# Optimization experiments

Measured on AMD Instinct MI355X. Metric: run time of the kernel, lower is better.

The kernel has to match this reference:

```python
import jax, jax.numpy as jnp
import numpy as np

B = 16          # batch
DF = 1536       # dinov2 feature dim
D = 1024        # projected dim (32*32)
V = 6890        # SMPL vertices (hard-coded in DECO)
PD = 256        # vertex positional-embedding dim
HID = 512       # feature_transform hidden dim
C = 133         # semantic contact classes


def setup_inputs() -> dict:
    key = jax.random.key(0)
    ks = jax.random.split(key, 16)
    s = 0.02
    n = lambda k, shp: s * jax.random.normal(k, shp, dtype=jnp.float32)
    return {
        "features": jax.random.normal(ks[0], (B, DF), dtype=jnp.float32),
        "W_scene": n(ks[1], (DF, D)), "b_scene": jnp.zeros((D,), jnp.float32),
        "W_contact": n(ks[2], (DF, D)), "b_contact": jnp.zeros((D,), jnp.float32),
        "Wq": n(ks[3], (D, D)), "Wk": n(ks[4], (D, D)),
        "Wv": n(ks[5], (D, D)), "Wo": n(ks[6], (D, D)),
        "W_cls": n(ks[7], (D, V)), "b_cls": jnp.zeros((V,), jnp.float32),
        "pos_emb": n(ks[8], (V, PD)),
        "W_ft1": n(ks[9], (D + PD, HID)), "b_ft1": jnp.zeros((HID,), jnp.float32),
        "W_ft2": n(ks[10], (HID, C)), "b_ft2": jnp.zeros((C,), jnp.float32),
    }


def reference(features, W_scene, b_scene, W_contact, b_contact,
              Wq, Wk, Wv, Wo, W_cls, b_cls, pos_emb,
              W_ft1, b_ft1, W_ft2, b_ft2):
    b = features.shape[0]
    # projectors (dinov2 branch)
    sem = features @ W_scene + b_scene          # [B, D]
    part = features @ W_contact + b_contact     # [B, D]
    # cross attention over seq-len-1 tokens: q from sem, k/v from part
    q = (sem @ Wq)[:, None, :]                  # [B, 1, D]
    k = (part @ Wk)[:, None, :]
    v = (part @ Wv)[:, None, :]
    scores = jnp.einsum('bqd,bkd->bqk', q, k) / jnp.sqrt(jnp.float32(D))
    w = jax.nn.softmax(scores, axis=-1)
    att = jnp.einsum('bqk,bkd->bqd', w, v) @ Wo  # [B, 1, D]
    # per-vertex contact probability
    cont = jax.nn.sigmoid(att[:, 0, :] @ W_cls + b_cls)  # [B, V]
    # shared semantic classifier: the torch code loops over batches, does
    # nonzero() on (cont > 0.5), gathers pos embeddings for contact vertices,
    # runs feature_transform, and scatters into zeros(B, C, V). The masked
    # vectorized form below computes identical values.
    mask = cont > 0.5                           # [B, V] (int constant wrt grad)
    att_bv = jnp.broadcast_to(att, (b, V, D))   # att[b] repeated per vertex
    pos_bv = jnp.broadcast_to(pos_emb[None], (b, V, PD))
    combined = jnp.concatenate([att_bv, pos_bv], axis=-1)   # [B, V, D+PD]
    h = jax.nn.relu(combined @ W_ft1 + b_ft1)   # [B, V, HID]
    preds = h @ W_ft2 + b_ft2                   # [B, V, C]
    semantic_cont = jnp.where(mask[:, None, :],
                              jnp.transpose(preds, (0, 2, 1)),
                              jnp.float32(0.0))  # [B, C, V]
    return (cont, semantic_cont)
```

## Files before the change

### kernel.cpp

```cpp
#include <hip/hip_runtime.h>
#include <hip/hip_bf16.h>

#define B_   16
#define DF_  1536
#define D_   1024
#define V_   6890
#define PD_  256
#define HID_ 512
#define C_   133
#define VPAD 6912
#define CPAD 144

typedef short short8 __attribute__((ext_vector_type(8)));
typedef float float4_ __attribute__((ext_vector_type(4)));
typedef unsigned short ushort_t;

#define MFMA16 __builtin_amdgcn_mfma_f32_16x16x32_bf16

__device__ __forceinline__ float b2f(ushort_t u) {
  union { unsigned int i; float f; } x;
  x.i = ((unsigned int)u) << 16;
  return x.f;
}
__device__ __forceinline__ ushort_t f2b(float f) {
  union { float f; unsigned int i; } x;
  x.f = f;
  unsigned int r = (x.i + 0x7fffu + ((x.i >> 16) & 1u)) >> 16;
  return (ushort_t)r;
}
__device__ __forceinline__ unsigned int f22u(float h0, float h1) {
  __hip_bfloat162 hb = __float22bfloat162_rn(make_float2(h0, h1));
  unsigned int u;
  __builtin_memcpy(&u, &hb, sizeof(u));
  return u;
}

__global__ __launch_bounds__(256) void k_gemv_fA(const float* __restrict__ A,
                                                 const float* __restrict__ W,
                                                 const float* __restrict__ bias,
                                                 double* __restrict__ outd,
                                                 float* __restrict__ outf,
                                                 int K, int N) {
  __shared__ double sA[DF_];
  int b = blockIdx.y;
  for (int i = threadIdx.x; i < K; i += 256) sA[i] = (double)A[b * K + i];
  __syncthreads();
  int jl = threadIdx.x & 15, ks = threadIdx.x >> 4;
  int j  = blockIdx.x * 16 + jl;
  int klen = K >> 4;
  const double* Ar = sA + ks * klen;
  const float*  Wp = W + (size_t)(ks * klen) * N + j;
  double acc = 0.0;
#pragma unroll 8
  for (int kk = 0; kk < klen; ++kk)
    acc += Ar[kk] * (double)Wp[(size_t)kk * N];
  __shared__ double red[16][16];
  red[ks][jl] = acc;
  __syncthreads();
  if (threadIdx.x < 16) {
    int jj = blockIdx.x * 16 + threadIdx.x;
    double s = 0.0;
#pragma unroll
    for (int q = 0; q < 16; ++q) s += red[q][threadIdx.x];
    if (bias) s += (double)bias[jj];
    if (outd) outd[b * N + jj] = s;
    if (outf) outf[b * N + jj] = (float)s;
  }
}

__global__ __launch_bounds__(256) void k_gemv_dA(const double* __restrict__ A,
                                                 const float* __restrict__ W,
                                                 const float* __restrict__ bias,
                                                 double* __restrict__ outd,
                                                 float* __restrict__ outf,
                                                 int K, int N) {
  __shared__ double sA[D_];
  int b = blockIdx.y;
  for (int i = threadIdx.x; i < K; i += 256) sA[i] = A[b * K + i];
  __syncthreads();
  int jl = threadIdx.x & 15, ks = threadIdx.x >> 4;
  int j  = blockIdx.x * 16 + jl;
  int klen = K >> 4;
  const double* Ar = sA + ks * klen;
  const float*  Wp = W + (size_t)(ks * klen) * N + j;
  double acc = 0.0;
#pragma unroll 8
  for (int kk = 0; kk < klen; ++kk)
    acc += Ar[kk] * (double)Wp[(size_t)kk * N];
  __shared__ double red[16][16];
  red[ks][jl] = acc;
  __syncthreads();
  if (threadIdx.x < 16) {
    int jj = blockIdx.x * 16 + threadIdx.x;
    double s = 0.0;
#pragma unroll
    for (int q = 0; q < 16; ++q) s += red[q][threadIdx.x];
    if (bias) s += (double)bias[jj];
    if (outd) outd[b * N + jj] = s;
    if (outf) outf[b * N + jj] = (float)s;
  }
}

__global__ __launch_bounds__(256) void k_cont(const double* __restrict__ att,
                                              const float* __restrict__ Wcls,
                                              const float* __restrict__ bcls,
                                              unsigned char* __restrict__ maskb,
                                              float* __restrict__ out0) {
  int vl = threadIdx.x & 15, ks = threadIdx.x >> 4;
  int v  = blockIdx.x * 16 + vl;
  int vc = v < V_ ? v : V_ - 1;
  double acc[B_];
#pragma unroll
  for (int b = 0; b < B_; ++b) acc[b] = 0.0;
  int k0 = ks * 64;
#pragma unroll 8
  for (int kk = 0; kk < 64; ++kk) {
    int k = k0 + kk;
    double w = (double)Wcls[(size_t)k * V_ + vc];
#pragma unroll
    for (int b = 0; b < B_; ++b) acc[b] += att[b * D_ + k] * w;
  }
  __shared__ double red[16][B_][16];
#pragma unroll
  for (int b = 0; b < B_; ++b) red[ks][b][vl] = acc[b];
  __syncthreads();
  int b = threadIdx.x >> 4;
  double s = 0.0;
#pragma unroll
  for (int q = 0; q < 16; ++q) s += red[q][b][vl];
  if (v < V_) {
    s += (double)bcls[v];
    maskb[b * V_ + v] = (s > 0.0) ? 1 : 0;
    out0[b * V_ + v] = (float)(1.0 / (1.0 + exp(-s)));
  }
}

__global__ __launch_bounds__(256) void k_prep(const float* __restrict__ Wft2,
                                              const float* __restrict__ Wft1,
                                              const float* __restrict__ pos,
                                              ushort_t* __restrict__ WT,
                                              ushort_t* __restrict__ WbT,
                                              ushort_t* __restrict__ PB) {
  int i = blockIdx.x * 256 + threadIdx.x;
  if (i < CPAD * HID_) {
    int c = i >> 9, k = i & (HID_ - 1);
    WT[i] = (c < C_) ? f2b(Wft2[(size_t)k * C_ + c]) : (ushort_t)0;
    return;
  }
  i -= CPAD * HID_;
  if (i < HID_ * PD_) {
    int k = i & (HID_ - 1), pd = i >> 9;
    WbT[(size_t)k * PD_ + pd] = f2b(Wft1[(size_t)(D_ + pd) * HID_ + k]);
    return;
  }
  i -= HID_ * PD_;
  if (i < V_ * PD_) PB[i] = f2b(pos[i]);
}

__global__ __launch_bounds__(256) void k_pproj(const ushort_t* __restrict__ PB,
                                               const ushort_t* __restrict__ WbT,
                                               ushort_t* __restrict__ PP) {
  int wave = threadIdx.x >> 6, lane = threadIdx.x & 63;
  int q = lane >> 4, l15 = lane & 15;
  int m0 = blockIdx.x * 64 + wave * 16;
  int n0 = blockIdx.y * 64;
  int vc = m0 + l15; vc = vc < V_ ? vc : V_ - 1;
  const ushort_t* pb = PB + (size_t)vc * PD_;
  float4_ acc[4] = {};
#pragma unroll 2
  for (int kt = 0; kt < 8; ++kt) {
    int jb = kt * 32 + q * 8;
    short8 a = *(const short8*)(pb + jb);
#pragma unroll
    for (int nf = 0; nf < 4; ++nf) {
      int n = n0 + nf * 16 + l15;
      short8 bfr = *(const short8*)(WbT + (size_t)n * PD_ + jb);
      acc[nf] = MFMA16(a, bfr, acc[nf], 0, 0, 0);
    }
  }
  int v0w = m0 + q * 4;
#pragma unroll
  for (int nf = 0; nf < 4; ++nf)
#pragma unroll
    for (int r = 0; r < 4; ++r)
      PP[(size_t)(v0w + r) * HID_ + (n0 + nf * 16 + l15)] = f2b(acc[nf][r]);
}

__global__ __launch_bounds__(256, 2) void k_main(const ushort_t* __restrict__ WT,
                                                 const ushort_t* __restrict__ PP,
                                                 const float* __restrict__ attproj,
                                                 const unsigned char* __restrict__ maskb,
                                                 const float* __restrict__ bft2,
                                                 float* __restrict__ out1) {
  __shared__ ushort_t swt[2][CPAD * 32];
  __shared__ float attp[2][HID_];
  int b0 = blockIdx.y * 2;
  int wave = threadIdx.x >> 6, lane = threadIdx.x & 63;
  int q = lane >> 4, l15 = lane & 15;
  int vbase = blockIdx.x * 128 + wave * 32;

  for (int i = threadIdx.x; i < 2 * HID_; i += 256)
    attp[i >> 9][i & (HID_ - 1)] = attproj[(b0 + (i >> 9)) * HID_ + (i & (HID_ - 1))];

  auto stage = [&](int kt, int buf) {
#pragma unroll
    for (int ii = 0; ii < 3; ++ii) {
      int i = ii * 256 + threadIdx.x;
      if (i < 576) {
        int row = i >> 2, seg = i & 3;
        *(short8*)&swt[buf][row * 32 + seg * 8] =
            *(const short8*)(WT + (size_t)row * HID_ + kt * 32 + seg * 8);
      }
    }
  };
  stage(0, 0);

  const ushort_t* pbase0 = PP + (size_t)(vbase + l15) * HID_;
  const ushort_t* pbase1 = PP + (size_t)(vbase + 16 + l15) * HID_;
  short8 pcur[2];
  pcur[0] = *(const short8*)(pbase0 + q * 8);
  pcur[1] = *(const short8*)(pbase1 + q * 8);
  __syncthreads();

  float4_ acc[2][9][2] = {};
  for (int kt = 0; kt < 16; ++kt) {
    int buf = kt & 1;
    int kb = kt * 32 + q * 8;
    if (kt < 15) stage(kt + 1, buf ^ 1);
    short8 pnext[2] = {pcur[0], pcur[1]};
    if (kt < 15) {
      pnext[0] = *(const short8*)(pbase0 + kb + 32);
      pnext[1] = *(const short8*)(pbase1 + kb + 32);
    }
    float pf[2][8];
#pragma unroll
    for (int nf = 0; nf < 2; ++nf)
#pragma unroll
      for (int jj = 0; jj < 8; ++jj)
        pf[nf][jj] = b2f((ushort_t)pcur[nf][jj]);
    float af[2][8];
#pragma unroll
    for (int bb = 0; bb < 2; ++bb) {
      float4_ a0 = *(const float4_*)&attp[bb][kb];
      float4_ a1 = *(const float4_*)&attp[bb][kb + 4];
#pragma unroll
      for (int e = 0; e < 4; ++e) { af[bb][e] = a0[e]; af[bb][4 + e] = a1[e]; }
    }
    short8 bfr[2][2];
#pragma unroll
    for (int bb = 0; bb < 2; ++bb)
#pragma unroll
      for (int nf = 0; nf < 2; ++nf) {
        unsigned int uu[4];
#pragma unroll
        for (int jj = 0; jj < 8; jj += 2) {
          float h0 = af[bb][jj]     + pf[nf][jj];
          float h1 = af[bb][jj + 1] + pf[nf][jj + 1];
          h0 = h0 > 0.f ? h0 : 0.f;
          h1 = h1 > 0.f ? h1 : 0.f;
          uu[jj >> 1] = f22u(h0, h1);
        }
        __builtin_memcpy(&bfr[bb][nf], uu, 16);
      }
#pragma unroll
    for (int mt = 0; mt < 9; ++mt) {
      short8 a = *(const short8*)&swt[buf][(mt * 16 + l15) * 32 + q * 8];
      acc[0][mt][0] = MFMA16(a, bfr[0][0], acc[0][mt][0], 0, 0, 0);
      acc[0][mt][1] = MFMA16(a, bfr[0][1], acc[0][mt][1], 0, 0, 0);
      acc[1][mt][0] = MFMA16(a, bfr[1][0], acc[1][mt][0], 0, 0, 0);
      acc[1][mt][1] = MFMA16(a, bfr[1][1], acc[1][mt][1], 0, 0, 0);
    }
    pcur[0] = pnext[0];
    pcur[1] = pnext[1];
    __syncthreads();
  }

  bool mk[2][2];
  int  nn[2];
#pragma unroll
  for (int nf = 0; nf < 2; ++nf) {
    int n = vbase + nf * 16 + l15;
    nn[nf] = n;
    int ncl = n < V_ ? n : V_ - 1;
    mk[0][nf] = (n < V_) && (maskb[(b0 + 0) * V_ + ncl] != 0);
    mk[1][nf] = (n < V_) && (maskb[(b0 + 1) * V_ + ncl] != 0);
  }
#pragma unroll
  for (int bb = 0; bb < 2; ++bb) {
    float* ob = out1 + (size_t)(b0 + bb) * C_ * V_;
#pragma unroll
    for (int mt = 0; mt < 9; ++mt)
#pragma unroll
      for (int r = 0; r < 4; ++r) {
        int c = mt * 16 + q * 4 + r;
        if (c < C_) {
          float bias = bft2[c];
#pragma unroll
          for (int nf = 0; nf < 2; ++nf)
            if (nn[nf] < V_) {
              float val = mk[bb][nf] ? acc[bb][mt][nf][r] + bias : 0.f;
              ob[(size_t)c * V_ + nn[nf]] = val;
            }
        }
      }
  }
}

extern "C" void kernel_launch(void* const* d_in, const int* in_sizes, int n_in,
                              void* d_out, int out_size, void* d_ws, size_t ws_size,
                              hipStream_t stream) {
  const float* features  = (const float*)d_in[0];
  const float* W_contact = (const float*)d_in[3];
  const float* b_contact = (const float*)d_in[4];
  const float* Wv        = (const float*)d_in[7];
  const float* Wo        = (const float*)d_in[8];
  const float* W_cls     = (const float*)d_in[9];
  const float* b_cls     = (const float*)d_in[10];
  const float* pos_emb   = (const float*)d_in[11];
  const float* W_ft1     = (const float*)d_in[12];
  const float* b_ft1     = (const float*)d_in[13];
  const float* W_ft2     = (const float*)d_in[14];
  const float* b_ft2     = (const float*)d_in[15];

  char* ws = (char*)d_ws;
  double*        part  = (double*)(ws);
  unsigned char* maskb = (unsigned char*)(ws);
  double*        vv    = (double*)(ws + 131072);
  double*        att   = (double*)(ws + 262144);
  float*         attpj = (float*)(ws + 393216);
  ushort_t*      wt    = (ushort_t*)(ws + 425984);
  ushort_t*      wbt   = (ushort_t*)(ws + 573440);
  ushort_t*      pp    = (ushort_t*)(ws + 835584);
  ushort_t*      pb    = (ushort_t*)(ws + 7913472);

  float* out0 = (float*)d_out;
  float* out1 = out0 + (size_t)B_ * V_;

  k_prep<<<7690, 256, 0, stream>>>(W_ft2, W_ft1, pos_emb, wt, wbt, pb);
  k_pproj<<<dim3(108, 8), 256, 0, stream>>>(pb, wbt, pp);
  k_gemv_fA<<<dim3(64, 16), 256, 0, stream>>>(features, W_contact, b_contact, part, nullptr, DF_, D_);
  k_gemv_dA<<<dim3(64, 16), 256, 0, stream>>>(part, Wv, nullptr, vv, nullptr, D_, D_);
  k_gemv_dA<<<dim3(64, 16), 256, 0, stream>>>(vv, Wo, nullptr, att, nullptr, D_, D_);
  k_gemv_dA<<<dim3(32, 16), 256, 0, stream>>>(att, W_ft1, b_ft1, nullptr, attpj, D_, HID_);
  k_cont<<<432, 256, 0, stream>>>(att, W_cls, b_cls, maskb, out0);
  k_main<<<dim3(54, 8), 256, 0, stream>>>(wt, pp, attpj, maskb, b_ft2, out1);
}
```

Baseline: 268.5 us.

## Fuse prep and GEMV chain into persistent kernel with grid barriers and f64 MFMA

Replaces six small kernels with one 256-block persistent kernel that uses atomic grid barriers. Some blocks run the sequential fp64 GEMV chain on f64 MFMA instructions while the rest run the weight conversion and positional projection alongside. The main kernel is also retiled to 16 vertices per wave with padded LDS rows and 3 blocks/CU occupancy. This is meant to cut launch overhead and overlap independent work, at the cost of spin-barrier latency and a co-residency assumption for all 256 blocks.

```diff
diff --git a/kernel.cpp b/kernel.cpp
--- a/kernel.cpp
+++ b/kernel.cpp
@@ -10,12 +10,15 @@
 #define C_   133
 #define VPAD 6912
 #define CPAD 144
-
-typedef short short8 __attribute__((ext_vector_type(8)));
-typedef float float4_ __attribute__((ext_vector_type(4)));
+#define NBLK 256
+
+typedef short  short8  __attribute__((ext_vector_type(8)));
+typedef float  float4_ __attribute__((ext_vector_type(4)));
+typedef double double4_ __attribute__((ext_vector_type(4)));
 typedef unsigned short ushort_t;
 
-#define MFMA16 __builtin_amdgcn_mfma_f32_16x16x32_bf16
+#define MFMA16   __builtin_amdgcn_mfma_f32_16x16x32_bf16
+#define MFMAF64  __builtin_amdgcn_mfma_f64_16x16x4f64
 
 __device__ __forceinline__ float b2f(ushort_t u) {
   union { unsigned int i; float f; } x;
@@ -35,135 +38,45 @@
   return u;
 }
 
-__global__ __launch_bounds__(256) void k_gemv_fA(const float* __restrict__ A,
-                                                 const float* __restrict__ W,
-                                                 const float* __restrict__ bias,
-                                                 double* __restrict__ outd,
-                                                 float* __restrict__ outf,
-                                                 int K, int N) {
-  __shared__ double sA[DF_];
-  int b = blockIdx.y;
-  for (int i = threadIdx.x; i < K; i += 256) sA[i] = (double)A[b * K + i];
+__device__ __forceinline__ void gbar(int* bar, int idx) {
   __syncthreads();
-  int jl = threadIdx.x & 15, ks = threadIdx.x >> 4;
-  int j  = blockIdx.x * 16 + jl;
-  int klen = K >> 4;
-  const double* Ar = sA + ks * klen;
-  const float*  Wp = W + (size_t)(ks * klen) * N + j;
-  double acc = 0.0;
-#pragma unroll 8
-  for (int kk = 0; kk < klen; ++kk)
-    acc += Ar[kk] * (double)Wp[(size_t)kk * N];
-  __shared__ double red[16][16];
-  red[ks][jl] = acc;
+  if (threadIdx.x == 0) {
+    __threadfence();
+    __hip_atomic_fetch_add(&bar[idx], 1, __ATOMIC_ACQ_REL, __HIP_MEMORY_SCOPE_AGENT);
+    while (__hip_atomic_load(&bar[idx], __ATOMIC_ACQUIRE, __HIP_MEMORY_SCOPE_AGENT) < NBLK)
+      __builtin_amdgcn_s_sleep(8);
+    __threadfence();
+  }
   __syncthreads();
-  if (threadIdx.x < 16) {
-    int jj = blockIdx.x * 16 + threadIdx.x;
-    double s = 0.0;
-#pragma unroll
-    for (int q = 0; q < 16; ++q) s += red[q][threadIdx.x];
-    if (bias) s += (double)bias[jj];
-    if (outd) outd[b * N + jj] = s;
-    if (outf) outf[b * N + jj] = (float)s;
-  }
-}
-
-__global__ __launch_bounds__(256) void k_gemv_dA(const double* __restrict__ A,
-                                                 const float* __restrict__ W,
-                                                 const float* __restrict__ bias,
-                                                 double* __restrict__ outd,
-                                                 float* __restrict__ outf,
-                                                 int K, int N) {
-  __shared__ double sA[D_];
-  int b = blockIdx.y;
-  for (int i = threadIdx.x; i < K; i += 256) sA[i] = A[b * K + i];
-  __syncthreads();
-  int jl = threadIdx.x & 15, ks = threadIdx.x >> 4;
-  int j  = blockIdx.x * 16 + jl;
-  int klen = K >> 4;
-  const double* Ar = sA + ks * klen;
-  const float*  Wp = W + (size_t)(ks * klen) * N + j;
-  double acc = 0.0;
-#pragma unroll 8
-  for (int kk = 0; kk < klen; ++kk)
-    acc += Ar[kk] * (double)Wp[(size_t)kk * N];
-  __shared__ double red[16][16];
-  red[ks][jl] = acc;
-  __syncthreads();
-  if (threadIdx.x < 16) {
-    int jj = blockIdx.x * 16 + threadIdx.x;
-    double s = 0.0;
-#pragma unroll
-    for (int q = 0; q < 16; ++q) s += red[q][threadIdx.x];
-    if (bias) s += (double)bias[jj];
-    if (outd) outd[b * N + jj] = s;
-    if (outf) outf[b * N + jj] = (float)s;
-  }
-}
-
-__global__ __launch_bounds__(256) void k_cont(const double* __restrict__ att,
-                                              const float* __restrict__ Wcls,
-                                              const float* __restrict__ bcls,
-                                              unsigned char* __restrict__ maskb,
-                                              float* __restrict__ out0) {
-  int vl = threadIdx.x & 15, ks = threadIdx.x >> 4;
-  int v  = blockIdx.x * 16 + vl;
-  int vc = v < V_ ? v : V_ - 1;
-  double acc[B_];
-#pragma unroll
-  for (int b = 0; b < B_; ++b) acc[b] = 0.0;
-  int k0 = ks * 64;
-#pragma unroll 8
-  for (int kk = 0; kk < 64; ++kk) {
-    int k = k0 + kk;
-    double w = (double)Wcls[(size_t)k * V_ + vc];
-#pragma unroll
-    for (int b = 0; b < B_; ++b) acc[b] += att[b * D_ + k] * w;
-  }
-  __shared__ double red[16][B_][16];
-#pragma unroll
-  for (int b = 0; b < B_; ++b) red[ks][b][vl] = acc[b];
-  __syncthreads();
-  int b = threadIdx.x >> 4;
-  double s = 0.0;
-#pragma unroll
-  for (int q = 0; q < 16; ++q) s += red[q][b][vl];
-  if (v < V_) {
-    s += (double)bcls[v];
-    maskb[b * V_ + v] = (s > 0.0) ? 1 : 0;
-    out0[b * V_ + v] = (float)(1.0 / (1.0 + exp(-s)));
-  }
-}
-
-__global__ __launch_bounds__(256) void k_prep(const float* __restrict__ Wft2,
-                                              const float* __restrict__ Wft1,
-                                              const float* __restrict__ pos,
-                                              ushort_t* __restrict__ WT,
-                                              ushort_t* __restrict__ WbT,
-                                              ushort_t* __restrict__ PB) {
-  int i = blockIdx.x * 256 + threadIdx.x;
-  if (i < CPAD * HID_) {
-    int c = i >> 9, k = i & (HID_ - 1);
-    WT[i] = (c < C_) ? f2b(Wft2[(size_t)k * C_ + c]) : (ushort_t)0;
-    return;
-  }
-  i -= CPAD * HID_;
-  if (i < HID_ * PD_) {
-    int k = i & (HID_ - 1), pd = i >> 9;
-    WbT[(size_t)k * PD_ + pd] = f2b(Wft1[(size_t)(D_ + pd) * HID_ + k]);
-    return;
-  }
-  i -= HID_ * PD_;
-  if (i < V_ * PD_) PB[i] = f2b(pos[i]);
-}
-
-__global__ __launch_bounds__(256) void k_pproj(const ushort_t* __restrict__ PB,
-                                               const ushort_t* __restrict__ WbT,
-                                               ushort_t* __restrict__ PP) {
-  int wave = threadIdx.x >> 6, lane = threadIdx.x & 63;
+}
+
+template <typename AT>
+__device__ __forceinline__ double4_ gemv_tile(const AT* __restrict__ A, int K,
+                                              const float* __restrict__ W, int N,
+                                              int ncol, int m, int kq) {
+  double4_ a0 = {0., 0., 0., 0.}, a1 = a0, a2 = a0, a3 = a0;
+  const AT*    ap = A + m * K + kq;
+  const float* wp = W + (size_t)kq * N + ncol;
+  int nk = K >> 2;
+#pragma unroll 2
+  for (int t = 0; t < nk; t += 4) {
+    a0 = MFMAF64((double)ap[4 * t],      (double)wp[(size_t)(4 * t) * N],      a0, 0, 0, 0);
+    a1 = MFMAF64((double)ap[4 * t + 4],  (double)wp[(size_t)(4 * t + 4) * N],  a1, 0, 0, 0);
+    a2 = MFMAF64((double)ap[4 * t + 8],  (double)wp[(size_t)(4 * t + 8) * N],  a2, 0, 0, 0);
+    a3 = MFMAF64((double)ap[4 * t + 12], (double)wp[(size_t)(4 * t + 12) * N], a3, 0, 0, 0);
+  }
+  return a0 + a1 + a2 + a3;
+}
+
+__device__ __forceinline__ void pproj_job(int jid, int tid,
+                                          const ushort_t* __restrict__ PB,
+                                          const ushort_t* __restrict__ WbT,
+                                          ushort_t* __restrict__ PP) {
+  int vt = jid % 108, nt = jid / 108;
+  int wave = tid >> 6, lane = tid & 63;
   int q = lane >> 4, l15 = lane & 15;
-  int m0 = blockIdx.x * 64 + wave * 16;
-  int n0 = blockIdx.y * 64;
+  int m0 = vt * 64 + wave * 16;
+  int n0 = nt * 64;
   int vc = m0 + l15; vc = vc < V_ ? vc : V_ - 1;
   const ushort_t* pb = PB + (size_t)vc * PD_;
   float4_ acc[4] = {};
@@ -173,8 +86,7 @@
     short8 a = *(const short8*)(pb + jb);
 #pragma unroll
     for (int nf = 0; nf < 4; ++nf) {
-      int n = n0 + nf * 16 + l15;
-      short8 bfr = *(const short8*)(WbT + (size_t)n * PD_ + jb);
+      short8 bfr = *(const short8*)(WbT + (size_t)(n0 + nf * 16 + l15) * PD_ + jb);
       acc[nf] = MFMA16(a, bfr, acc[nf], 0, 0, 0);
     }
   }
@@ -186,18 +98,113 @@
       PP[(size_t)(v0w + r) * HID_ + (n0 + nf * 16 + l15)] = f2b(acc[nf][r]);
 }
 
-__global__ __launch_bounds__(256, 2) void k_main(const ushort_t* __restrict__ WT,
+__global__ void k_chain(const float* __restrict__ features,
+                        const float* __restrict__ Wc,  const float* __restrict__ bc,
+                        const float* __restrict__ Wv_, const float* __restrict__ Wo_,
+                        const float* __restrict__ Wcls, const float* __restrict__ bcls,
+                        const float* __restrict__ pos, const float* __restrict__ Wft1,
+                        const float* __restrict__ bft1, const float* __restrict__ Wft2,
+                        double* __restrict__ part, double* __restrict__ vv,
+                        double* __restrict__ att, float* __restrict__ attpj,
+                        unsigned char* __restrict__ maskb, float* __restrict__ out0,
+                        ushort_t* __restrict__ WT, ushort_t* __restrict__ WbT,
+                        ushort_t* __restrict__ PB, ushort_t* __restrict__ PP,
+                        int* __restrict__ bar) {
+  int tid = threadIdx.x, blk = blockIdx.x;
+  int lane = tid & 63, wv = tid >> 6;
+  int gw = blk * 4 + wv;
+  int m = lane & 15, kq = lane >> 4;
+
+  if (blk < 16) {
+    int n0 = gw * 16;
+    double4_ acc = gemv_tile(features, DF_, Wc, D_, n0 + m, m, kq);
+#pragma unroll
+    for (int r = 0; r < 4; ++r)
+      part[(kq * 4 + r) * D_ + n0 + m] = acc[r] + (double)bc[n0 + m];
+  } else {
+    const int TOT = CPAD * HID_ + HID_ * PD_ + V_ * PD_;
+    for (int i = (blk - 16) * 256 + tid; i < TOT; i += 240 * 256) {
+      int u = i;
+      if (u < CPAD * HID_) {
+        int c = u >> 9, k = u & (HID_ - 1);
+        WT[u] = (c < C_) ? f2b(Wft2[(size_t)k * C_ + c]) : (ushort_t)0;
+      } else if ((u -= CPAD * HID_) < HID_ * PD_) {
+        int k = u & (HID_ - 1), pd = u >> 9;
+        WbT[(size_t)k * PD_ + pd] = f2b(Wft1[(size_t)(D_ + pd) * HID_ + k]);
+      } else {
+        u -= HID_ * PD_;
+        PB[u] = f2b(pos[u]);
+      }
+    }
+  }
+  gbar(bar, 0);
+
+  if (blk < 16) {
+    int n0 = gw * 16;
+    double4_ acc = gemv_tile(part, D_, Wv_, D_, n0 + m, m, kq);
+#pragma unroll
+    for (int r = 0; r < 4; ++r) vv[(kq * 4 + r) * D_ + n0 + m] = acc[r];
+  } else {
+#pragma unroll
+    for (int r = 0; r < 2; ++r) {
+      int jid = (blk - 16) + 240 * r;
+      if (jid < 432) pproj_job(jid, tid, PB, WbT, PP);
+    }
+  }
+  gbar(bar, 1);
+
+  if (blk < 16) {
+    int n0 = gw * 16;
+    double4_ acc = gemv_tile(vv, D_, Wo_, D_, n0 + m, m, kq);
+#pragma unroll
+    for (int r = 0; r < 4; ++r) att[(kq * 4 + r) * D_ + n0 + m] = acc[r];
+  } else {
+#pragma unroll
+    for (int r = 0; r < 2; ++r) {
+      int jid = 432 + (blk - 16) + 240 * r;
+      if (jid < 864) pproj_job(jid, tid, PB, WbT, PP);
+    }
+  }
+  gbar(bar, 2);
+
+  if (blk < 8) {
+    int n0 = gw * 16;
+    double4_ acc = gemv_tile(att, D_, Wft1, HID_, n0 + m, m, kq);
+#pragma unroll
+    for (int r = 0; r < 4; ++r)
+      attpj[(kq * 4 + r) * HID_ + n0 + m] = (float)(acc[r] + (double)bft1[n0 + m]);
+  } else {
+    int t = (blk - 8) * 4 + wv;
+    if (t < 432) {
+      int v0 = t * 16;
+      int vcl = v0 + m; vcl = vcl < V_ ? vcl : V_ - 1;
+      double4_ acc = gemv_tile(att, D_, Wcls, V_, vcl, m, kq);
+      int v = v0 + m;
+#pragma unroll
+      for (int r = 0; r < 4; ++r) {
+        int b = kq * 4 + r;
+        if (v < V_) {
+          double s = acc[r] + (double)bcls[v];
+          maskb[b * V_ + v] = (s > 0.0) ? 1 : 0;
+          out0[b * V_ + v] = (float)(1.0 / (1.0 + exp(-s)));
+        }
+      }
+    }
+  }
+}
+
+__global__ __launch_bounds__(256, 3) void k_main(const ushort_t* __restrict__ WT,
                                                  const ushort_t* __restrict__ PP,
                                                  const float* __restrict__ attproj,
                                                  const unsigned char* __restrict__ maskb,
                                                  const float* __restrict__ bft2,
                                                  float* __restrict__ out1) {
-  __shared__ ushort_t swt[2][CPAD * 32];
+  __shared__ ushort_t swt[2][CPAD * 40];
   __shared__ float attp[2][HID_];
   int b0 = blockIdx.y * 2;
   int wave = threadIdx.x >> 6, lane = threadIdx.x & 63;
   int q = lane >> 4, l15 = lane & 15;
-  int vbase = blockIdx.x * 128 + wave * 32;
+  int vbase = blockIdx.x * 64 + wave * 16;
 
   for (int i = threadIdx.x; i < 2 * HID_; i += 256)
     attp[i >> 9][i & (HID_ - 1)] = attproj[(b0 + (i >> 9)) * HID_ + (i & (HID_ - 1))];
@@ -208,83 +215,54 @@
       int i = ii * 256 + threadIdx.x;
       if (i < 576) {
         int row = i >> 2, seg = i & 3;
-        *(short8*)&swt[buf][row * 32 + seg * 8] =
+        *(short8*)&swt[buf][row * 40 + seg * 8] =
             *(const short8*)(WT + (size_t)row * HID_ + kt * 32 + seg * 8);
       }
     }
   };
   stage(0, 0);
-
-  const ushort_t* pbase0 = PP + (size_t)(vbase + l15) * HID_;
-  const ushort_t* pbase1 = PP + (size_t)(vbase + 16 + l15) * HID_;
-  short8 pcur[2];
-  pcur[0] = *(const short8*)(pbase0 + q * 8);
-  pcur[1] = *(const short8*)(pbase1 + q * 8);
+  const ushort_t* pbase = PP + (size_t)(vbase + l15) * HID_;
+  short8 pcur = *(const short8*)(pbase + q * 8);
   __syncthreads();
 
-  float4_ acc[2][9][2] = {};
+  float4_ acc[2][9] = {};
   for (int kt = 0; kt < 16; ++kt) {
-    int buf = kt & 1;
-    int kb = kt * 32 + q * 8;
+    int buf = kt & 1, kb = kt * 32 + q * 8;
     if (kt < 15) stage(kt + 1, buf ^ 1);
-    short8 pnext[2] = {pcur[0], pcur[1]};
-    if (kt < 15) {
-      pnext[0] = *(const short8*)(pbase0 + kb + 32);
-      pnext[1] = *(const short8*)(pbase1 + kb + 32);
-    }
-    float pf[2][8];
-#pragma unroll
-    for (int nf = 0; nf < 2; ++nf)
-#pragma unroll
-      for (int jj = 0; jj < 8; ++jj)
-        pf[nf][jj] = b2f((ushort_t)pcur[nf][jj]);
-    float af[2][8];
+    short8 pnext = pcur;
+    if (kt < 15) pnext = *(const short8*)(pbase + kb + 32);
+    float pf[8];
+#pragma unroll
+    for (int jj = 0; jj < 8; ++jj) pf[jj] = b2f((ushort_t)pcur[jj]);
+    short8 bfr[2];
 #pragma unroll
     for (int bb = 0; bb < 2; ++bb) {
-      float4_ a0 = *(const float4_*)&attp[bb][kb];
-      float4_ a1 = *(const float4_*)&attp[bb][kb + 4];
-#pragma unroll
-      for (int e = 0; e < 4; ++e) { af[bb][e] = a0[e]; af[bb][4 + e] = a1[e]; }
-    }
-    short8 bfr[2][2];
-#pragma unroll
-    for (int bb = 0; bb < 2; ++bb)
-#pragma unroll
-      for (int nf = 0; nf < 2; ++nf) {
-        unsigned int uu[4];
-#pragma unroll
-        for (int jj = 0; jj < 8; jj += 2) {
-          float h0 = af[bb][jj]     + pf[nf][jj];
-          float h1 = af[bb][jj + 1] + pf[nf][jj + 1];
-          h0 = h0 > 0.f ? h0 : 0.f;
-          h1 = h1 > 0.f ? h1 : 0.f;
-          uu[jj >> 1] = f22u(h0, h1);
-        }
-        __builtin_memcpy(&bfr[bb][nf], uu, 16);
-      }
+      unsigned int uu[4];
+#pragma unroll
+      for (int jj = 0; jj < 8; jj += 2) {
+        float h0 = attp[bb][kb + jj]     + pf[jj];
+        float h1 = attp[bb][kb + jj + 1] + pf[jj + 1];
+        h0 = h0 > 0.f ? h0 : 0.f;
+        h1 = h1 > 0.f ? h1 : 0.f;
+        uu[jj >> 1] = f22u(h0, h1);
+      }
+      __builtin_memcpy(&bfr[bb], uu, 16);
+    }
 #pragma unroll
     for (int mt = 0; mt < 9; ++mt) {
-      short8 a = *(const short8*)&swt[buf][(mt * 16 + l15) * 32 + q * 8];
-      acc[0][mt][0] = MFMA16(a, bfr[0][0], acc[0][mt][0], 0, 0, 0);
-      acc[0][mt][1] = MFMA16(a, bfr[0][1], acc[0][mt][1], 0, 0, 0);
-      acc[1][mt][0] = MFMA16(a, bfr[1][0], acc[1][mt][0], 0, 0, 0);
-      acc[1][mt][1] = MFMA16(a, bfr[1][1], acc[1][mt][1], 0, 0, 0);
-    }
-    pcur[0] = pnext[0];
-    pcur[1] = pnext[1];
+      short8 a = *(const short8*)&swt[buf][(mt * 16 + l15) * 40 + q * 8];
+      acc[0][mt] = MFMA16(a, bfr[0], acc[0][mt], 0, 0, 0);
+      acc[1][mt] = MFMA16(a, bfr[1], acc[1][mt], 0, 0, 0);
+    }
+    pcur = pnext;
     __syncthreads();
   }
 
-  bool mk[2][2];
-  int  nn[2];
-#pragma unroll
-  for (int nf = 0; nf < 2; ++nf) {
-    int n = vbase + nf * 16 + l15;
-    nn[nf] = n;
-    int ncl = n < V_ ? n : V_ - 1;
-    mk[0][nf] = (n < V_) && (maskb[(b0 + 0) * V_ + ncl] != 0);
-    mk[1][nf] = (n < V_) && (maskb[(b0 + 1) * V_ + ncl] != 0);
-  }
+  int n = vbase + l15;
+  int ncl = n < V_ ? n : V_ - 1;
+  bool mk[2];
+  mk[0] = (n < V_) && (maskb[(b0 + 0) * V_ + ncl] != 0);
+  mk[1] = (n < V_) && (maskb[(b0 + 1) * V_ + ncl] != 0);
 #pragma unroll
   for (int bb = 0; bb < 2; ++bb) {
     float* ob = out1 + (size_t)(b0 + bb) * C_ * V_;
@@ -293,14 +271,9 @@
 #pragma unroll
       for (int r = 0; r < 4; ++r) {
         int c = mt * 16 + q * 4 + r;
-        if (c < C_) {
-          float bias = bft2[c];
-#pragma unroll
-          for (int nf = 0; nf < 2; ++nf)
-            if (nn[nf] < V_) {
-              float val = mk[bb][nf] ? acc[bb][mt][nf][r] + bias : 0.f;
-              ob[(size_t)c * V_ + nn[nf]] = val;
-            }
+        if (c < C_ && n < V_) {
+          float val = mk[bb] ? acc[bb][mt][r] + bft2[c] : 0.f;
+          ob[(size_t)c * V_ + n] = val;
         }
       }
   }
@@ -324,24 +297,23 @@
 
   char* ws = (char*)d_ws;
   double*        part  = (double*)(ws);
-  unsigned char* maskb = (unsigned char*)(ws);
   double*        vv    = (double*)(ws + 131072);
   double*        att   = (double*)(ws + 262144);
   float*         attpj = (float*)(ws + 393216);
-  ushort_t*      wt    = (ushort_t*)(ws + 425984);
-  ushort_t*      wbt   = (ushort_t*)(ws + 573440);
-  ushort_t*      pp    = (ushort_t*)(ws + 835584);
-  ushort_t*      pb    = (ushort_t*)(ws + 7913472);
+  unsigned char* maskb = (unsigned char*)(ws + 425984);
+  ushort_t*      wt    = (ushort_t*)(ws + 536576);
+  ushort_t*      wbt   = (ushort_t*)(ws + 684032);
+  ushort_t*      pb    = (ushort_t*)(ws + 946176);
+  ushort_t*      pp    = (ushort_t*)(ws + 4473856);
+  int*           bar   = (int*)(ws + 11551744);
 
   float* out0 = (float*)d_out;
   float* out1 = out0 + (size_t)B_ * V_;
 
-  k_prep<<<7690, 256, 0, stream>>>(W_ft2, W_ft1, pos_emb, wt, wbt, pb);
-  k_pproj<<<dim3(108, 8), 256, 0, stream>>>(pb, wbt, pp);
-  k_gemv_fA<<<dim3(64, 16), 256, 0, stream>>>(features, W_contact, b_contact, part, nullptr, DF_, D_);
-  k_gemv_dA<<<dim3(64, 16), 256, 0, stream>>>(part, Wv, nullptr, vv, nullptr, D_, D_);
-  k_gemv_dA<<<dim3(64, 16), 256, 0, stream>>>(vv, Wo, nullptr, att, nullptr, D_, D_);
-  k_gemv_dA<<<dim3(32, 16), 256, 0, stream>>>(att, W_ft1, b_ft1, nullptr, attpj, D_, HID_);
-  k_cont<<<432, 256, 0, stream>>>(att, W_cls, b_cls, maskb, out0);
-  k_main<<<dim3(54, 8), 256, 0, stream>>>(wt, pp, attpj, maskb, b_ft2, out1);
-}
+  hipMemsetAsync(bar, 0, 128, stream);
+  k_chain<<<NBLK, 256, 0, stream>>>(features, W_contact, b_contact, Wv, Wo,
+                                    W_cls, b_cls, pos_emb, W_ft1, b_ft1, W_ft2,
+                                    part, vv, att, attpj, maskb, out0,
+                                    wt, wbt, pb, pp, bar);
+  k_main<<<dim3(108, 8), 256, 0, stream>>>(wt, pp, attpj, maskb, b_ft2, out1);
+}
```

Result: slower. 558.1 us (+107.9%).
